# Performance work log

Hardware: AMD Instinct MI355X
Metric: run time of the kernel (lower is better)

## Reference

```python
import jax, jax.numpy as jnp
import numpy as np

DIM, HEADS, LAYERS, HID = 1024, 16, 6, 4096
PAST_CTX, MAX_PERIOD = 1000, 10000.0
HEAD_DIM = DIM // HEADS


def _ln(x, g, b, eps=1e-5):
    m = jnp.mean(x, axis=-1, keepdims=True)
    v = jnp.mean((x - m) ** 2, axis=-1, keepdims=True)
    return (x - m) * jax.lax.rsqrt(v + eps) * g + b


def setup_inputs() -> dict:
    key = jax.random.key(0)
    ks = jax.random.split(key, 8)
    s = 0.02
    inp = {
        "x": jax.random.normal(ks[0], (2, 2048, DIM), jnp.float32),
        "norm_in_g": jnp.ones((DIM,), jnp.float32),
        "norm_in_b": jnp.zeros((DIM,), jnp.float32),
        "Wqkv": jax.random.normal(ks[1], (LAYERS, 3 * DIM, DIM), jnp.float32) * s,
        "bqkv": jnp.zeros((LAYERS, 3 * DIM), jnp.float32),
        "Wo": jax.random.normal(ks[2], (LAYERS, DIM, DIM), jnp.float32) * s,
        "bo": jnp.zeros((LAYERS, DIM), jnp.float32),
        "ln1_g": jnp.ones((LAYERS, DIM), jnp.float32),
        "ln1_b": jnp.zeros((LAYERS, DIM), jnp.float32),
        "ln2_g": jnp.ones((LAYERS, DIM), jnp.float32),
        "ln2_b": jnp.zeros((LAYERS, DIM), jnp.float32),
        "W1": jax.random.normal(ks[3], (LAYERS, HID, DIM), jnp.float32) * s,
        "b1": jnp.zeros((LAYERS, HID), jnp.float32),
        "W2": jax.random.normal(ks[4], (LAYERS, DIM, HID), jnp.float32) * s,
        "b2": jnp.zeros((LAYERS, DIM), jnp.float32),
    }
    return inp


def _forward(x, norm_in_g, norm_in_b, Wqkv, bqkv, Wo, bo, ln1_g, ln1_b, ln2_g, ln2_b, W1, b1, W2, b2):
    B, T, C = x.shape
    H = 1  # states=None -> per-layer zero cache of length 1
    # sinusoidal positional embedding (offset=0)
    half = C // 2
    positions = jnp.arange(T, dtype=jnp.float32)[None, :, None]  # [1,T,1]
    adim = jnp.arange(half, dtype=jnp.float32)[None, None, :]
    phase = positions / (MAX_PERIOD ** (adim / (half - 1)))
    pos_emb = jnp.concatenate([jnp.cos(phase), jnp.sin(phase)], axis=-1)  # [1,T,C]
    x = _ln(x, norm_in_g, norm_in_b) + pos_emb

    # sliding-window causal mask over keys [past(H) | current(T)]
    q_pos = jnp.arange(H, T + H)[:, None]
    k_pos = jnp.arange(T + H)[None, :]
    delta = q_pos - k_pos
    valid = (delta >= 0) & (delta <= PAST_CTX)  # [T, T+H]
    neg = jnp.finfo(x.dtype).min

    past = jnp.zeros((B, H, C), x.dtype)
    for l in range(LAYERS):
        # post-norm layer (norm_first=False)
        keys = jnp.concatenate([past, x], axis=1)  # [B,T+H,C]
        Wq, Wk, Wv = Wqkv[l][:C], Wqkv[l][C:2 * C], Wqkv[l][2 * C:]
        bq, bk, bv = bqkv[l][:C], bqkv[l][C:2 * C], bqkv[l][2 * C:]
        q = (x @ Wq.T + bq).reshape(B, T, HEADS, HEAD_DIM)
        k = (keys @ Wk.T + bk).reshape(B, T + H, HEADS, HEAD_DIM)
        v = (keys @ Wv.T + bv).reshape(B, T + H, HEADS, HEAD_DIM)
        scores = jnp.einsum('bqhd,bkhd->bhqk', q, k) / jnp.sqrt(jnp.asarray(HEAD_DIM, x.dtype))
        scores = jnp.where(valid[None, None], scores, neg)
        attn = jax.nn.softmax(scores, axis=-1)
        o = jnp.einsum('bhqk,bkhd->bqhd', attn, v).reshape(B, T, C)
        o = o @ Wo[l].T + bo[l]
        x = _ln(x + o, ln1_g[l], ln1_b[l])
        ff = jax.nn.gelu(x @ W1[l].T + b1[l], approximate=False) @ W2[l].T + b2[l]
        x = _ln(x + ff, ln2_g[l], ln2_b[l])
    return x


def reference(x, norm_in_g, norm_in_b, Wqkv, bqkv, Wo, bo, ln1_g, ln1_b, ln2_g, ln2_b, W1, b1, W2, b2):
    return _forward(x, norm_in_g, norm_in_b, Wqkv, bqkv, Wo, bo, ln1_g, ln1_b, ln2_g, ln2_b, W1, b1, W2, b2)
```

## Files before the change

### kernel.cpp

```cpp
#include <hip/hip_runtime.h>
#include <math.h>

typedef short short8 __attribute__((ext_vector_type(8)));
typedef float floatx4 __attribute__((ext_vector_type(4)));

__device__ __forceinline__ unsigned short f2bf(float f) {
  unsigned int u = __builtin_bit_cast(unsigned int, f);
  u = (u + 0x7FFFu + ((u >> 16) & 1u)) >> 16;
  return (unsigned short)u;
}

__device__ __forceinline__ unsigned int pack_bf2(float lo, float hi) {
  return (unsigned int)f2bf(lo) | ((unsigned int)f2bf(hi) << 16);
}

__device__ __forceinline__ void async16(const void* g, void* l) {
  __builtin_amdgcn_global_load_lds(
      (const __attribute__((address_space(1))) unsigned int*)g,
      (__attribute__((address_space(3))) unsigned int*)l, 16, 0, 0);
}

template <int EPI, int BM>
__global__ __launch_bounds__(512, 2) void gemm3(
    const unsigned short* __restrict__ A, const unsigned short* __restrict__ B,
    const float* __restrict__ bias, void* __restrict__ outp,
    int M, int N, int K) {
  constexpr int BN = 128;
  constexpr int ROWS = BM + BN;
  constexpr int BUFE = ROWS * 64;
  constexpr int NLT = ROWS / 64;
  constexpr int WM = BM / 64;
  constexpr int WN = 8 / WM;
  constexpr int NJ = (BN / WN) / 16;
  __shared__ unsigned short S[3 * BUFE];

  const int tid = threadIdx.x;
  const int lane = tid & 63, wid = tid >> 6;
  const int quad = lane >> 4, l15 = lane & 15;
  const int wm = wid / WN, wn = wid % WN;
  const int wmo = wm * 64;
  const int wno = wn * (BN / WN);

  const int gx = gridDim.x;
  const int nwg = gx * gridDim.y;
  int lin = blockIdx.y * gx + blockIdx.x;
  lin = (lin & 7) * (nwg >> 3) + (lin >> 3);
  const size_t m0 = (size_t)(lin / gx) * BM;
  const size_t n0 = (size_t)(lin % gx) * BN;

  auto stage = [&](int buf, int kt) {
#pragma unroll
    for (int l = 0; l < NLT; ++l) {
      int ci = l * 512 + tid;
      int r = ci >> 3;
      int c = (ci & 7) ^ (r & 7);
      const unsigned short* src =
          (r < BM) ? A + (m0 + r) * (size_t)K + kt + c * 8
                   : B + (n0 + (r - BM)) * (size_t)K + kt + c * 8;
      async16(src, &S[buf * BUFE + ci * 8]);
    }
  };

  floatx4 acc[4][NJ] = {};

  stage(0, 0);
  stage(1, 64);
  int cur = 0;

  for (int kt = 0; kt < K; kt += 64) {
    if (kt + 128 < K) {
      int nb = cur + 2;
      if (nb >= 3) nb -= 3;
      stage(nb, kt + 128);
      asm volatile("s_waitcnt vmcnt(%0)" ::"n"(2 * NLT) : "memory");
    } else if (kt + 64 < K) {
      asm volatile("s_waitcnt vmcnt(%0)" ::"n"(NLT) : "memory");
    } else {
      asm volatile("s_waitcnt vmcnt(0)" ::: "memory");
    }
    __builtin_amdgcn_s_barrier();
    __builtin_amdgcn_sched_barrier(0);

    short8 a[4][2], b[NJ][2];
    const unsigned short* Sc = &S[cur * BUFE];
#pragma unroll
    for (int i = 0; i < 4; ++i) {
      const int R = wmo + i * 16 + l15;
#pragma unroll
      for (int kh = 0; kh < 2; ++kh)
        a[i][kh] = *(const short8*)&Sc[R * 64 + (((kh * 4 + quad) ^ (R & 7)) * 8)];
    }
#pragma unroll
    for (int j = 0; j < NJ; ++j) {
      const int R = BM + wno + j * 16 + l15;
#pragma unroll
      for (int kh = 0; kh < 2; ++kh)
        b[j][kh] = *(const short8*)&Sc[R * 64 + (((kh * 4 + quad) ^ (R & 7)) * 8)];
    }
    asm volatile("s_waitcnt lgkmcnt(0)" ::: "memory");
    __builtin_amdgcn_sched_barrier(0);
    __builtin_amdgcn_s_barrier();

    __builtin_amdgcn_s_setprio(1);
#pragma unroll
    for (int kh = 0; kh < 2; ++kh)
#pragma unroll
      for (int i = 0; i < 4; ++i)
#pragma unroll
        for (int j = 0; j < NJ; ++j)
          acc[i][j] = __builtin_amdgcn_mfma_f32_16x16x32_bf16(
              a[i][kh], b[j][kh], acc[i][j], 0, 0, 0);
    __builtin_amdgcn_s_setprio(0);

    ++cur;
    if (cur >= 3) cur -= 3;
  }

#pragma unroll
  for (int j = 0; j < NJ; ++j) {
    const int n = (int)n0 + wno + j * 16 + l15;
    const float bv = bias[n];
    const float sc = (EPI == 3 && n < 1024) ? 0.125f : 1.0f;
#pragma unroll
    for (int i = 0; i < 4; ++i) {
      const int mbase = (int)m0 + wmo + i * 16 + quad * 4;
#pragma unroll
      for (int r = 0; r < 4; ++r) {
        float v = acc[i][j][r] + bv;
        if (EPI == 2) v = 0.5f * v * (1.0f + erff(v * 0.70710678f));
        if (EPI == 3) v *= sc;
        size_t idx = (size_t)(mbase + r) * (size_t)N + n;
        if (EPI == 1) ((float*)outp)[idx] = v;
        else ((unsigned short*)outp)[idx] = f2bf(v);
      }
    }
  }
}

__global__ __launch_bounds__(512) void attn_kernel(
    const unsigned short* __restrict__ qkv, const float* __restrict__ bqkv_l,
    unsigned short* __restrict__ attno) {
  __shared__ unsigned short Qs[128 * 64];
  __shared__ unsigned short Ks[2][64 * 64];
  __shared__ unsigned short Vrow[2][64 * 64];
  __shared__ unsigned short Vt[64 * 72];
  __shared__ unsigned short Ps[8][16 * 72];
  __shared__ float Lsh[8][16];

  const int qt = blockIdx.x, h = blockIdx.y, b = blockIdx.z;
  const int qs = qt * 128;
  const int tid = threadIdx.x, lane = tid & 63, wid = tid >> 6;
  const int quad = lane >> 4, l15 = lane & 15;
  const size_t rowbase = (size_t)b * 2048;
  const int hoff = h * 64;

#pragma unroll
  for (int r = 0; r < 2; ++r) {
    int c = r * 512 + tid;
    int qrow = c >> 3, ccq = c & 7;
    async16(qkv + (rowbase + qs + qrow) * 3072 + hoff + ((ccq ^ (qrow & 7)) * 8),
            &Qs[c * 8]);
  }

  floatx4 oacc[4] = {};
  float lpart = 0.f;

  int kstart = qs - 999;
  if (kstart < 0) kstart = 0;
  kstart &= ~63;
  const int kend = qs + 128;

  const int krow = tid >> 3, cc = tid & 7;
  const int qlo = qs + wid * 16 + 1;
  const int qhi = qlo + 15;
  const int qpos = qs + wid * 16 + l15 + 1;

  auto stageKV = [&](int buf, int k0) {
    int xr = k0 + krow - 1;
    xr = xr < 0 ? 0 : (xr > 2047 ? 2047 : xr);
    async16(qkv + (rowbase + xr) * 3072 + 1024 + hoff + ((cc ^ (krow & 7)) * 8),
            &Ks[buf][tid * 8]);
    async16(qkv + (rowbase + xr) * 3072 + 2048 + hoff + cc * 8,
            &Vrow[buf][tid * 8]);
  };

  stageKV(0, kstart);
  int cur = 0;

  for (int k0 = kstart; k0 <= kend; k0 += 64) {
    if (k0 + 64 <= kend) {
      stageKV(cur ^ 1, k0 + 64);
      asm volatile("s_waitcnt vmcnt(2)" ::: "memory");
    } else {
      asm volatile("s_waitcnt vmcnt(0)" ::: "memory");
    }
    __builtin_amdgcn_s_barrier();
    __builtin_amdgcn_sched_barrier(0);

    if (k0 == 0) {
      if (tid < 64) Ks[cur][tid] = f2bf(bqkv_l[1024 + hoff + tid]);
      __syncthreads();
    }

    {
      short8 vv = *(const short8*)&Vrow[cur][tid * 8];
#pragma unroll
      for (int e = 0; e < 8; ++e) {
        int e2 = (e + cc) & 7;
        Vt[(cc * 8 + e2) * 72 + krow] = (unsigned short)vv[e2];
      }
      if (k0 == 0 && tid < 64) Vt[tid * 72] = f2bf(bqkv_l[2048 + hoff + tid]);
    }

    const bool act = (k0 <= qhi) && (qlo - (k0 + 63) <= 1000);
    if (act) {
      floatx4 sacc[4] = {};
#pragma unroll
      for (int ks = 0; ks < 2; ++ks) {
        short8 bq = *(const short8*)&Qs[(wid * 16 + l15) * 64 +
                                        (((ks * 4 + quad) ^ (l15 & 7)) * 8)];
#pragma unroll
        for (int nj = 0; nj < 4; ++nj) {
          short8 ak = *(const short8*)&Ks[cur][(nj * 16 + l15) * 64 +
                                              (((ks * 4 + quad) ^ (l15 & 7)) * 8)];
          sacc[nj] = __builtin_amdgcn_mfma_f32_16x16x32_bf16(ak, bq, sacc[nj], 0, 0, 0);
        }
      }

      const bool full = (k0 + 63 <= qlo) && (qhi - k0 <= 1000);
#pragma unroll
      for (int nj = 0; nj < 4; ++nj) {
        float e[4];
        if (full) {
#pragma unroll
          for (int r = 0; r < 4; ++r) e[r] = __expf(sacc[nj][r]);
        } else {
          const int keyb = k0 + nj * 16 + quad * 4;
#pragma unroll
          for (int r = 0; r < 4; ++r) {
            int delta = qpos - (keyb + r);
            e[r] = (delta >= 0 && delta <= 1000) ? __expf(sacc[nj][r]) : 0.f;
          }
        }
        lpart += (e[0] + e[1]) + (e[2] + e[3]);
        uint2 pk = make_uint2(pack_bf2(e[0], e[1]), pack_bf2(e[2], e[3]));
        *(uint2*)&Ps[wid][l15 * 72 + nj * 16 + quad * 4] = pk;
      }
    }

    asm volatile("s_waitcnt lgkmcnt(0)" ::: "memory");
    __builtin_amdgcn_sched_barrier(0);
    __builtin_amdgcn_s_barrier();
    __builtin_amdgcn_sched_barrier(0);

    if (act) {
#pragma unroll
      for (int ks = 0; ks < 2; ++ks) {
        short8 pf = *(const short8*)&Ps[wid][l15 * 72 + ks * 32 + quad * 8];
#pragma unroll
        for (int di = 0; di < 4; ++di) {
          short8 vf = *(const short8*)&Vt[(di * 16 + l15) * 72 + ks * 32 + quad * 8];
          oacc[di] = __builtin_amdgcn_mfma_f32_16x16x32_bf16(pf, vf, oacc[di], 0, 0, 0);
        }
      }
    }
    cur ^= 1;
  }

  lpart += __shfl_xor(lpart, 16);
  lpart += __shfl_xor(lpart, 32);
  if (quad == 0) Lsh[wid][l15] = lpart;
  __builtin_amdgcn_s_waitcnt(0);
  float linv[4];
#pragma unroll
  for (int r = 0; r < 4; ++r) linv[r] = 1.0f / Lsh[wid][quad * 4 + r];

#pragma unroll
  for (int di = 0; di < 4; ++di)
#pragma unroll
    for (int r = 0; r < 4; ++r) {
      int q = qs + wid * 16 + quad * 4 + r;
      attno[(rowbase + q) * 1024 + hoff + di * 16 + l15] =
          f2bf(oacc[di][r] * linv[r]);
    }
}

__global__ __launch_bounds__(256) void ln_first_kernel(
    const float* __restrict__ xin, const float* __restrict__ g,
    const float* __restrict__ bb, float* __restrict__ xout,
    unsigned short* __restrict__ xbout) {
  const int row = blockIdx.x, tid = threadIdx.x;
  const size_t base = (size_t)row * 1024 + tid * 4;
  float4 xv = *(const float4*)&xin[base];
  float s = xv.x + xv.y + xv.z + xv.w;
  float sq = xv.x * xv.x + xv.y * xv.y + xv.z * xv.z + xv.w * xv.w;
  __shared__ float red[8];
  for (int off = 32; off > 0; off >>= 1) { s += __shfl_down(s, off); sq += __shfl_down(sq, off); }
  if ((tid & 63) == 0) { red[tid >> 6] = s; red[4 + (tid >> 6)] = sq; }
  __syncthreads();
  s = red[0] + red[1] + red[2] + red[3];
  sq = red[4] + red[5] + red[6] + red[7];
  const float mean = s * (1.f / 1024.f);
  const float rstd = rsqrtf(sq * (1.f / 1024.f) - mean * mean + 1e-5f);
  float4 gv = *(const float4*)&g[tid * 4];
  float4 bv = *(const float4*)&bb[tid * 4];
  const float tf = (float)(row & 2047);
  float xs[4] = {xv.x, xv.y, xv.z, xv.w};
  float gs[4] = {gv.x, gv.y, gv.z, gv.w};
  float bs[4] = {bv.x, bv.y, bv.z, bv.w};
  float y[4];
#pragma unroll
  for (int e = 0; e < 4; ++e) {
    int c = tid * 4 + e;
    float a = (c < 512) ? (float)c : (float)(c - 512);
    float ph = tf * powf(10000.f, -a * (1.f / 511.f));
    float pe = (c < 512) ? cosf(ph) : sinf(ph);
    y[e] = (xs[e] - mean) * rstd * gs[e] + bs[e] + pe;
  }
  *(float4*)&xout[base] = make_float4(y[0], y[1], y[2], y[3]);
  *(ushort4*)&xbout[base] = make_ushort4(f2bf(y[0]), f2bf(y[1]), f2bf(y[2]), f2bf(y[3]));
}

__global__ __launch_bounds__(256) void ln_res_kernel(
    const float* __restrict__ xin, const float* __restrict__ addv,
    const float* __restrict__ g, const float* __restrict__ bb,
    float* __restrict__ xout, unsigned short* __restrict__ xbout) {
  const int row = blockIdx.x, tid = threadIdx.x;
  const size_t base = (size_t)row * 1024 + tid * 4;
  float4 xv = *(const float4*)&xin[base];
  float4 av = *(const float4*)&addv[base];
  float v0 = xv.x + av.x, v1 = xv.y + av.y, v2 = xv.z + av.z, v3 = xv.w + av.w;
  float s = v0 + v1 + v2 + v3;
  float sq = v0 * v0 + v1 * v1 + v2 * v2 + v3 * v3;
  __shared__ float red[8];
  for (int off = 32; off > 0; off >>= 1) { s += __shfl_down(s, off); sq += __shfl_down(sq, off); }
  if ((tid & 63) == 0) { red[tid >> 6] = s; red[4 + (tid >> 6)] = sq; }
  __syncthreads();
  s = red[0] + red[1] + red[2] + red[3];
  sq = red[4] + red[5] + red[6] + red[7];
  const float mean = s * (1.f / 1024.f);
  const float rstd = rsqrtf(sq * (1.f / 1024.f) - mean * mean + 1e-5f);
  float4 gv = *(const float4*)&g[tid * 4];
  float4 bv = *(const float4*)&bb[tid * 4];
  float vs[4] = {v0, v1, v2, v3};
  float gs[4] = {gv.x, gv.y, gv.z, gv.w};
  float bs[4] = {bv.x, bv.y, bv.z, bv.w};
  float y[4];
#pragma unroll
  for (int e = 0; e < 4; ++e) y[e] = (vs[e] - mean) * rstd * gs[e] + bs[e];
  *(float4*)&xout[base] = make_float4(y[0], y[1], y[2], y[3]);
  if (xbout)
    *(ushort4*)&xbout[base] = make_ushort4(f2bf(y[0]), f2bf(y[1]), f2bf(y[2]), f2bf(y[3]));
}

__global__ __launch_bounds__(256) void convw_kernel(
    const float* __restrict__ wqkv, const float* __restrict__ wo,
    const float* __restrict__ w1, const float* __restrict__ w2,
    unsigned short* __restrict__ dst) {
  for (int base = blockIdx.x * 256 + threadIdx.x; base < 3145728; base += 786432) {
    int i = base << 2;
    const float* src;
    int off;
    if (i < 3145728)      { src = wqkv; off = i; }
    else if (i < 4194304) { src = wo;   off = i - 3145728; }
    else if (i < 8388608) { src = w1;   off = i - 4194304; }
    else                  { src = w2;   off = i - 8388608; }
    float4 v = *(const float4*)&src[off];
    *(ushort4*)&dst[i] = make_ushort4(f2bf(v.x), f2bf(v.y), f2bf(v.z), f2bf(v.w));
  }
}

extern "C" void kernel_launch(void* const* d_in, const int* in_sizes, int n_in,
                              void* d_out, int out_size, void* d_ws, size_t ws_size,
                              hipStream_t stream) {
  const float* x    = (const float*)d_in[0];
  const float* ng   = (const float*)d_in[1];
  const float* nb   = (const float*)d_in[2];
  const float* Wqkv = (const float*)d_in[3];
  const float* bqkv = (const float*)d_in[4];
  const float* Wo   = (const float*)d_in[5];
  const float* bo   = (const float*)d_in[6];
  const float* ln1g = (const float*)d_in[7];
  const float* ln1b = (const float*)d_in[8];
  const float* ln2g = (const float*)d_in[9];
  const float* ln2b = (const float*)d_in[10];
  const float* W1   = (const float*)d_in[11];
  const float* b1   = (const float*)d_in[12];
  const float* W2   = (const float*)d_in[13];
  const float* b2   = (const float*)d_in[14];

  char* ws = (char*)d_ws;
  float* xf           = (float*)(ws + 0);
  unsigned short* xb  = (unsigned short*)(ws + 16777216);
  unsigned short* qkv = (unsigned short*)(ws + 25165824);
  unsigned short* att = (unsigned short*)(ws + 50331648);
  unsigned short* h1  = (unsigned short*)(ws + 58720256);
  float* gout         = (float*)(ws + 92274688);
  unsigned short* wb  = (unsigned short*)(ws + 109051904);
  unsigned short* wqkvb = wb;
  unsigned short* wob   = wb + 3145728;
  unsigned short* w1b   = wb + 4194304;
  unsigned short* w2b   = wb + 8388608;

  ln_first_kernel<<<4096, 256, 0, stream>>>(x, ng, nb, xf, xb);

  for (int l = 0; l < 6; ++l) {
    convw_kernel<<<3072, 256, 0, stream>>>(Wqkv + (size_t)l * 3145728,
                                           Wo + (size_t)l * 1048576,
                                           W1 + (size_t)l * 4194304,
                                           W2 + (size_t)l * 4194304, wb);
    gemm3<3, 256><<<dim3(24, 16), 512, 0, stream>>>(xb, wqkvb, bqkv + l * 3072, qkv,
                                                    4096, 3072, 1024);
    attn_kernel<<<dim3(16, 16, 2), 512, 0, stream>>>(qkv, bqkv + l * 3072, att);
    gemm3<1, 128><<<dim3(8, 32), 512, 0, stream>>>(att, wob, bo + l * 1024, gout,
                                                   4096, 1024, 1024);
    ln_res_kernel<<<4096, 256, 0, stream>>>(xf, gout, ln1g + l * 1024, ln1b + l * 1024,
                                            xf, xb);
    gemm3<2, 256><<<dim3(32, 16), 512, 0, stream>>>(xb, w1b, b1 + l * 4096, h1,
                                                    4096, 4096, 1024);
    gemm3<1, 64 + 64><<<dim3(8, 32), 512, 0, stream>>>(h1, w2b, b2 + l * 1024, gout,
                                                       4096, 1024, 4096);
    ln_res_kernel<<<4096, 256, 0, stream>>>(xf, gout, ln2g + l * 1024, ln2b + l * 1024,
                                            (l == 5) ? (float*)d_out : xf,
                                            (l == 5) ? nullptr : xb);
  }
}
```

Before: 1.739 ms.

## Restructure GEMM k-loop to one barrier per step and hoist address math

The GEMM main loop now issues the LDS fragment reads first and the next async global-to-LDS stage after them. The vmcnt wait and a single barrier move to after the MFMA block, replacing the two barriers per k-step used before. Global source pointers and swizzled LDS read offsets are computed once before the loop and advanced incrementally, which removes per-iteration index arithmetic. The intent is to cut synchronisation stalls and scalar/vector ALU overhead around the MFMAs. The cost is more live registers for the pointers and offsets, which could pressure occupancy.

After: 1.688 ms. 3.0% less time.

```diff
diff --git a/kernel.cpp b/kernel.cpp
--- a/kernel.cpp
+++ b/kernel.cpp
@@ -48,58 +48,69 @@
   const size_t m0 = (size_t)(lin / gx) * BM;
   const size_t n0 = (size_t)(lin % gx) * BN;
 
-  auto stage = [&](int buf, int kt) {
+  const unsigned short* sp[NLT];
+  unsigned ldst[NLT];
+#pragma unroll
+  for (int l = 0; l < NLT; ++l) {
+    int ci = l * 512 + tid;
+    int r = ci >> 3;
+    int c = (ci & 7) ^ (r & 7);
+    sp[l] = (r < BM ? A + (m0 + r) * (size_t)K
+                    : B + (n0 + (r - BM)) * (size_t)K) + c * 8;
+    ldst[l] = (unsigned)ci * 8;
+  }
+  auto stage = [&](int buf) {
 #pragma unroll
     for (int l = 0; l < NLT; ++l) {
-      int ci = l * 512 + tid;
-      int r = ci >> 3;
-      int c = (ci & 7) ^ (r & 7);
-      const unsigned short* src =
-          (r < BM) ? A + (m0 + r) * (size_t)K + kt + c * 8
-                   : B + (n0 + (r - BM)) * (size_t)K + kt + c * 8;
-      async16(src, &S[buf * BUFE + ci * 8]);
+      async16(sp[l], &S[buf * BUFE + ldst[l]]);
+      sp[l] += 64;
     }
   };
 
+  int aoff[4][2], boff[NJ][2];
+#pragma unroll
+  for (int i = 0; i < 4; ++i) {
+    const int R = wmo + i * 16 + l15;
+#pragma unroll
+    for (int kh = 0; kh < 2; ++kh)
+      aoff[i][kh] = R * 64 + (((kh * 4 + quad) ^ (R & 7)) * 8);
+  }
+#pragma unroll
+  for (int j = 0; j < NJ; ++j) {
+    const int R = BM + wno + j * 16 + l15;
+#pragma unroll
+    for (int kh = 0; kh < 2; ++kh)
+      boff[j][kh] = R * 64 + (((kh * 4 + quad) ^ (R & 7)) * 8);
+  }
+
   floatx4 acc[4][NJ] = {};
 
-  stage(0, 0);
-  stage(1, 64);
+  stage(0);
+  stage(1);
+  asm volatile("s_waitcnt vmcnt(%0)" ::"n"(NLT) : "memory");
+  __builtin_amdgcn_s_barrier();
+  __builtin_amdgcn_sched_barrier(0);
   int cur = 0;
 
   for (int kt = 0; kt < K; kt += 64) {
+    const unsigned short* Sc = &S[cur * BUFE];
+    short8 a[4][2], b[NJ][2];
+#pragma unroll
+    for (int i = 0; i < 4; ++i)
+#pragma unroll
+      for (int kh = 0; kh < 2; ++kh)
+        a[i][kh] = *(const short8*)&Sc[aoff[i][kh]];
+#pragma unroll
+    for (int j = 0; j < NJ; ++j)
+#pragma unroll
+      for (int kh = 0; kh < 2; ++kh)
+        b[j][kh] = *(const short8*)&Sc[boff[j][kh]];
+
     if (kt + 128 < K) {
       int nb = cur + 2;
       if (nb >= 3) nb -= 3;
-      stage(nb, kt + 128);
-      asm volatile("s_waitcnt vmcnt(%0)" ::"n"(2 * NLT) : "memory");
-    } else if (kt + 64 < K) {
-      asm volatile("s_waitcnt vmcnt(%0)" ::"n"(NLT) : "memory");
-    } else {
-      asm volatile("s_waitcnt vmcnt(0)" ::: "memory");
-    }
-    __builtin_amdgcn_s_barrier();
-    __builtin_amdgcn_sched_barrier(0);
-
-    short8 a[4][2], b[NJ][2];
-    const unsigned short* Sc = &S[cur * BUFE];
-#pragma unroll
-    for (int i = 0; i < 4; ++i) {
-      const int R = wmo + i * 16 + l15;
-#pragma unroll
-      for (int kh = 0; kh < 2; ++kh)
-        a[i][kh] = *(const short8*)&Sc[R * 64 + (((kh * 4 + quad) ^ (R & 7)) * 8)];
-    }
-#pragma unroll
-    for (int j = 0; j < NJ; ++j) {
-      const int R = BM + wno + j * 16 + l15;
-#pragma unroll
-      for (int kh = 0; kh < 2; ++kh)
-        b[j][kh] = *(const short8*)&Sc[R * 64 + (((kh * 4 + quad) ^ (R & 7)) * 8)];
-    }
-    asm volatile("s_waitcnt lgkmcnt(0)" ::: "memory");
-    __builtin_amdgcn_sched_barrier(0);
-    __builtin_amdgcn_s_barrier();
+      stage(nb);
+    }
 
     __builtin_amdgcn_s_setprio(1);
 #pragma unroll
@@ -111,6 +122,14 @@
           acc[i][j] = __builtin_amdgcn_mfma_f32_16x16x32_bf16(
               a[i][kh], b[j][kh], acc[i][j], 0, 0, 0);
     __builtin_amdgcn_s_setprio(0);
+
+    if (kt + 128 < K) {
+      asm volatile("s_waitcnt vmcnt(%0)" ::"n"(NLT) : "memory");
+    } else if (kt + 64 < K) {
+      asm volatile("s_waitcnt vmcnt(0)" ::: "memory");
+    }
+    __builtin_amdgcn_s_barrier();
+    __builtin_amdgcn_sched_barrier(0);
 
     ++cur;
     if (cur >= 3) cur -= 3;
@@ -418,8 +437,8 @@
                                             xf, xb);
     gemm3<2, 256><<<dim3(32, 16), 512, 0, stream>>>(xb, w1b, b1 + l * 4096, h1,
                                                     4096, 4096, 1024);
-    gemm3<1, 64 + 64><<<dim3(8, 32), 512, 0, stream>>>(h1, w2b, b2 + l * 1024, gout,
-                                                       4096, 1024, 4096);
+    gemm3<1, 128><<<dim3(8, 32), 512, 0, stream>>>(h1, w2b, b2 + l * 1024, gout,
+                                                   4096, 1024, 4096);
     ln_res_kernel<<<4096, 256, 0, stream>>>(xf, gout, ln2g + l * 1024, ln2b + l * 1024,
                                             (l == 5) ? (float*)d_out : xf,
                                             (l == 5) ? nullptr : xb);
```
